# Optimization experiments

Hardware: AMD Instinct MI355X
Metric: run time of the kernel (lower is better)

The kernel has to match this reference:

```python
import jax, jax.numpy as jnp
import numpy as np

B, S, E = 8, 4096, 2048
LATENT, HEAD = 64, 128


def setup_inputs() -> dict:
    key = jax.random.key(0)
    ks = jax.random.split(key, 5)
    sd = lambda n: 1.0 / np.sqrt(n)
    return {
        "x": jax.random.normal(ks[0], (B, S, E), dtype=jnp.float32),
        "w_dkv": jax.random.normal(ks[1], (E, LATENT), dtype=jnp.float32) * sd(E),
        "w_k": jax.random.normal(ks[2], (LATENT, HEAD), dtype=jnp.float32) * sd(LATENT),
        "w_v": jax.random.normal(ks[3], (LATENT, HEAD), dtype=jnp.float32) * sd(LATENT),
        "w_q": jax.random.normal(ks[4], (E, HEAD), dtype=jnp.float32) * sd(E),
    }


def reference(x, w_dkv, w_k, w_v, w_q):
    # x: [B,S,E]. kv_cache=None path: cache = fresh compressed latents.
    latent = jnp.einsum('bse,el->bsl', x, w_dkv)          # [B,S,latent] compressed KV cache
    k = jnp.einsum('bsl,lh->bsh', latent, w_k)            # decompress keys   [B,S,head]
    v = jnp.einsum('bsl,lh->bsh', latent, w_v)            # decompress values [B,S,head]
    q = jnp.einsum('bse,eh->bsh', x, w_q)                 # queries [B,S,head]
    scale = w_q.shape[-1] ** -0.5
    scores = jnp.einsum('bqh,bkh->bqk', q, k) * scale     # [B,S,S]
    seq = x.shape[1]
    causal = jnp.tril(jnp.ones((seq, seq), dtype=bool))   # tril(seq, cache_len)
    scores = jnp.where(causal, scores, -jnp.inf)
    attn = jax.nn.softmax(scores, axis=-1)                # dropout p=0 (eval)
    out = jnp.einsum('bqk,bkh->bqh', attn, v)             # [B,S,head]
    return out, latent
```

## Files before the change

kernel.cpp:

```cpp
#include <hip/hip_runtime.h>

typedef __bf16 bf16;
typedef __bf16 bf16x2 __attribute__((ext_vector_type(2)));
typedef __bf16 bf16x4 __attribute__((ext_vector_type(4)));
typedef __bf16 bf16x8 __attribute__((ext_vector_type(8)));
typedef float  f32x4  __attribute__((ext_vector_type(4)));

#define MFMA16(a,b,c) __builtin_amdgcn_mfma_f32_16x16x32_bf16((a),(b),(c),0,0,0)

constexpr int Bn = 8, Sn = 4096, En = 2048, Ln = 64, Hn = 128;
constexpr int Mrows = Bn * Sn;

__device__ __forceinline__ void load_lds_16(const bf16* g, bf16* l) {
    __builtin_amdgcn_global_load_lds(
        (const __attribute__((address_space(1))) uint32_t*)g,
        (__attribute__((address_space(3))) uint32_t*)l, 16, 0, 0);
}

__global__ __launch_bounds__(256) void transpose_cvt(const float* __restrict__ in,
                                                     bf16* __restrict__ out,
                                                     int K, int N) {
    int tid = blockIdx.x * 256 + threadIdx.x;
    if (tid >= K * N) return;
    int k = tid / N, n = tid - k * N;
    out[n * K + k] = (bf16)in[tid];
}

__global__ __launch_bounds__(512) void gemm_xw(const float* __restrict__ x,
                                               const bf16* __restrict__ wT,
                                               const bf16* __restrict__ wkT,
                                               const bf16* __restrict__ wvT,
                                               float* __restrict__ latent_out,
                                               bf16* __restrict__ q_out,
                                               bf16* __restrict__ k_out,
                                               bf16* __restrict__ vT_out) {
    __shared__ __align__(16) bf16 As[64 * 72];
    __shared__ __align__(16) bf16 Bs[192 * 64];
    const int lane = threadIdx.x & 63;
    const int wave = threadIdx.x >> 6;
    const int col  = lane & 15, quad = lane >> 4;
    const int mgrp  = wave >> 1;
    const int nhalf = wave & 1;
    const int mblock = blockIdx.x * 64;

    f32x4 acc[6];
#pragma unroll
    for (int t = 0; t < 6; ++t) acc[t] = (f32x4){0.f, 0.f, 0.f, 0.f};

    const int bsub = lane >> 3;
    const int bkg0 = lane & 7;
    const int akc  = threadIdx.x & 15;
    const int arow0 = threadIdx.x >> 4;

    for (int step = 0; step < 32; ++step) {
        __syncthreads();
#pragma unroll
        for (int j = 0; j < 3; ++j) {
            int nr0 = wave * 24 + j * 8;
            int n = nr0 + bsub;
            int kgrp = bkg0 ^ bsub;
            const bf16* g = wT + (size_t)n * En + step * 64 + kgrp * 8;
            load_lds_16(g, &Bs[nr0 * 64]);
        }
#pragma unroll
        for (int p = 0; p < 2; ++p) {
            int row = p * 32 + arow0;
            f32x4 v = *(const f32x4*)(x + (size_t)(mblock + row) * En + step * 64 + akc * 4);
            bf16x4 c;
#pragma unroll
            for (int j = 0; j < 4; ++j) c[j] = (bf16)v[j];
            *(bf16x4*)(&As[row * 72 + akc * 4]) = c;
        }
        __syncthreads();
#pragma unroll
        for (int ks2 = 0; ks2 < 2; ++ks2) {
            bf16x8 a = *(const bf16x8*)(&As[(mgrp * 16 + col) * 72 + ks2 * 32 + quad * 8]);
#pragma unroll
            for (int t = 0; t < 6; ++t) {
                int n = nhalf * 96 + t * 16 + col;
                int sg = (ks2 * 4 + quad) ^ (col & 7);
                bf16x8 b = *(const bf16x8*)(&Bs[n * 64 + sg * 8]);
                acc[t] = MFMA16(a, b, acc[t]);
            }
        }
    }
    __syncthreads();
    if (nhalf == 0) {
#pragma unroll
        for (int t = 0; t < 4; ++t)
#pragma unroll
            for (int r = 0; r < 4; ++r)
                As[(mgrp * 16 + quad * 4 + r) * 72 + t * 16 + col] = (bf16)acc[t][r];
    }
#pragma unroll
    for (int t = 0; t < 6; ++t) {
        int gnt = nhalf * 6 + t;
#pragma unroll
        for (int r = 0; r < 4; ++r) {
            int row = mblock + mgrp * 16 + quad * 4 + r;
            if (gnt < 4) latent_out[(size_t)row * Ln + gnt * 16 + col] = acc[t][r];
            else         q_out[(size_t)row * Hn + (gnt - 4) * 16 + col] = (bf16)acc[t][r];
        }
    }
    __syncthreads();
    const bf16* w2 = (nhalf == 0) ? wkT : wvT;
    f32x4 kv[8];
#pragma unroll
    for (int nt = 0; nt < 8; ++nt) kv[nt] = (f32x4){0.f, 0.f, 0.f, 0.f};
#pragma unroll
    for (int ks = 0; ks < 2; ++ks) {
        bf16x8 a = *(const bf16x8*)(&As[(mgrp * 16 + col) * 72 + ks * 32 + quad * 8]);
#pragma unroll
        for (int nt = 0; nt < 8; ++nt) {
            bf16x8 b = *(const bf16x8*)(w2 + (nt * 16 + col) * Ln + ks * 32 + quad * 8);
            kv[nt] = MFMA16(a, b, kv[nt]);
        }
    }
    if (nhalf == 0) {
#pragma unroll
        for (int nt = 0; nt < 8; ++nt)
#pragma unroll
            for (int r = 0; r < 4; ++r) {
                int row = mblock + mgrp * 16 + quad * 4 + r;
                k_out[(size_t)row * Hn + nt * 16 + col] = (bf16)kv[nt][r];
            }
    } else {
        int bb = mblock >> 12;
        int sbase = (mblock & 4095) + mgrp * 16 + quad * 4;
#pragma unroll
        for (int nt = 0; nt < 8; ++nt) {
            bf16x4 pv;
#pragma unroll
            for (int r = 0; r < 4; ++r) pv[r] = (bf16)kv[nt][r];
            *(bf16x4*)(vT_out + ((size_t)bb * Hn + nt * 16 + col) * Sn + sbase) = pv;
        }
    }
}

__global__ __launch_bounds__(256, 2) void mla_attn(const bf16* __restrict__ qg,
                                                   const bf16* __restrict__ kg,
                                                   const bf16* __restrict__ vtg,
                                                   float* __restrict__ outg) {
    __shared__ __align__(16) bf16 Ks[2][64 * 128];
    __shared__ __align__(16) bf16 VtS[2][128 * 64];
    __shared__ __align__(16) bf16 Pb[4][16][72];
    const int lane = threadIdx.x & 63;
    const int wave = threadIdx.x >> 6;
    const int col  = lane & 15, quad = lane >> 4;
    const int rank  = blockIdx.x;
    const int qtile = 63 - (rank >> 3);
    const int bb    = rank & 7;
    const int qbase = qtile * 64;
    const bf16* kb  = kg  + (size_t)bb * Sn * Hn;
    const bf16* vbT = vtg + (size_t)bb * Sn * Hn;

    bf16x8 qf[4];
    {
        const bf16* qrow = qg + ((size_t)bb * Sn + qbase + wave * 16 + col) * Hn;
#pragma unroll
        for (int ks = 0; ks < 4; ++ks)
            qf[ks] = *(const bf16x8*)(qrow + ks * 32 + quad * 8);
    }
    f32x4 o[8];
#pragma unroll
    for (int t = 0; t < 8; ++t) o[t] = (f32x4){0.f, 0.f, 0.f, 0.f};
    float m_run = -3.0e38f;
    float l_run = 0.f;
    const float scale = 0.08838834764831845f;
    const int qrow = wave * 16 + col;

    auto stage = [&](int buf, int kt_) {
#pragma unroll
        for (int ii = 0; ii < 4; ++ii) {
            int i = wave * 4 + ii;
            int key = 4 * i + (lane >> 4);
            int p = lane & 15;
            int g = (p & 8) | ((p & 7) ^ (key & 7));
            load_lds_16(kb + (size_t)(kt_ * 64 + key) * Hn + g * 8, &Ks[buf][i * 512]);
        }
#pragma unroll
        for (int ii = 0; ii < 4; ++ii) {
            int i = wave * 4 + ii;
            int r = i * 8 + (lane >> 3);
            int cs = (lane & 7) ^ (r & 7);
            load_lds_16(vbT + (size_t)r * Sn + kt_ * 64 + cs * 8, &VtS[buf][i * 512]);
        }
    };

    stage(0, 0);
    for (int kt = 0; kt <= qtile; ++kt) {
        const int cur = kt & 1;
        if (kt < qtile) {
            stage(cur ^ 1, kt + 1);
            asm volatile("s_waitcnt vmcnt(8)" ::: "memory");
        } else {
            asm volatile("s_waitcnt vmcnt(0)" ::: "memory");
        }
        __builtin_amdgcn_s_barrier();
        __builtin_amdgcn_sched_barrier(0);
        const bf16* KsC = Ks[cur];
        const bf16* VtC = VtS[cur];

        f32x4 sa[4];
#pragma unroll
        for (int nt = 0; nt < 4; ++nt) {
            sa[nt] = (f32x4){0.f, 0.f, 0.f, 0.f};
#pragma unroll
            for (int ks = 0; ks < 4; ++ks) {
                int key = nt * 16 + col;
                int g = ks * 4 + quad;
                int pos = (g & 8) | ((g & 7) ^ (col & 7));
                bf16x8 kfr = *(const bf16x8*)(KsC + key * 128 + pos * 8);
                sa[nt] = MFMA16(kfr, qf[ks], sa[nt]);
            }
        }
        float p_[4][4];
        if (kt == qtile) {
#pragma unroll
            for (int nt = 0; nt < 4; ++nt)
#pragma unroll
                for (int r = 0; r < 4; ++r) {
                    float s = sa[nt][r] * scale;
                    if (nt * 16 + quad * 4 + r > qrow) s = -1.0e30f;
                    p_[nt][r] = s;
                }
        } else {
#pragma unroll
            for (int nt = 0; nt < 4; ++nt)
#pragma unroll
                for (int r = 0; r < 4; ++r) p_[nt][r] = sa[nt][r] * scale;
        }
        float mt = p_[0][0];
#pragma unroll
        for (int nt = 0; nt < 4; ++nt)
#pragma unroll
            for (int r = 0; r < 4; ++r) mt = fmaxf(mt, p_[nt][r]);
        mt = fmaxf(mt, __shfl_xor(mt, 16, 64));
        mt = fmaxf(mt, __shfl_xor(mt, 32, 64));
        float mn = fmaxf(m_run, mt);
        float alpha = __expf(m_run - mn);
        m_run = mn;
        float rs = 0.f;
#pragma unroll
        for (int nt = 0; nt < 4; ++nt)
#pragma unroll
            for (int r = 0; r < 4; ++r) {
                float p = __expf(p_[nt][r] - mn);
                p_[nt][r] = p;
                rs += p;
            }
        rs += __shfl_xor(rs, 16, 64);
        rs += __shfl_xor(rs, 32, 64);
        l_run = l_run * alpha + rs;
        float al[4];
#pragma unroll
        for (int r = 0; r < 4; ++r) al[r] = __shfl(alpha, quad * 4 + r, 64);
#pragma unroll
        for (int t = 0; t < 8; ++t)
#pragma unroll
            for (int r = 0; r < 4; ++r) o[t][r] *= al[r];
#pragma unroll
        for (int nt = 0; nt < 4; ++nt) {
            bf16x4 pv;
#pragma unroll
            for (int r = 0; r < 4; ++r) pv[r] = (bf16)p_[nt][r];
            *(bf16x4*)(&Pb[wave][col][((nt ^ (col >> 2)) & 3) * 16 + quad * 4]) = pv;
        }
#pragma unroll
        for (int ks = 0; ks < 2; ++ks) {
            int pos = (ks * 32 + quad * 8) ^ ((col >> 2) * 16);
            bf16x8 pa = *(const bf16x8*)(&Pb[wave][col][pos]);
#pragma unroll
            for (int nt = 0; nt < 8; ++nt) {
                int row = nt * 16 + col;
                int g = (ks * 4 + quad) ^ (row & 7);
                bf16x8 bv = *(const bf16x8*)(VtC + row * 64 + g * 8);
                o[nt] = MFMA16(pa, bv, o[nt]);
            }
        }
        __builtin_amdgcn_sched_barrier(0);
        __builtin_amdgcn_s_barrier();
    }
    float lr[4];
#pragma unroll
    for (int r = 0; r < 4; ++r) lr[r] = __shfl(l_run, quad * 4 + r, 64);
#pragma unroll
    for (int r = 0; r < 4; ++r) {
        float inv = 1.0f / lr[r];
        int row = qbase + wave * 16 + quad * 4 + r;
        float* orow = outg + ((size_t)bb * Sn + row) * Hn;
#pragma unroll
        for (int t = 0; t < 8; ++t)
            orow[t * 16 + col] = o[t][r] * inv;
    }
}

extern "C" void kernel_launch(void* const* d_in, const int* in_sizes, int n_in,
                              void* d_out, int out_size, void* d_ws, size_t ws_size,
                              hipStream_t stream) {
    const float* x     = (const float*)d_in[0];
    const float* w_dkv = (const float*)d_in[1];
    const float* w_k   = (const float*)d_in[2];
    const float* w_v   = (const float*)d_in[3];
    const float* w_q   = (const float*)d_in[4];

    float* out        = (float*)d_out;
    float* latent_out = out + (size_t)Mrows * Hn;

    char* ws = (char*)d_ws;
    bf16* q_ws = (bf16*)(ws);
    bf16* k_ws = (bf16*)(ws + (size_t)8  * 1024 * 1024);
    bf16* v_ws = (bf16*)(ws + (size_t)16 * 1024 * 1024);
    bf16* wT   = (bf16*)(ws + (size_t)24 * 1024 * 1024);
    bf16* wkT  = (bf16*)(ws + (size_t)24 * 1024 * 1024 + 768 * 1024);
    bf16* wvT  = (bf16*)(ws + (size_t)24 * 1024 * 1024 + 784 * 1024);

    transpose_cvt<<<(En * Ln + 255) / 256, 256, 0, stream>>>(w_dkv, wT, En, Ln);
    transpose_cvt<<<(En * Hn + 255) / 256, 256, 0, stream>>>(w_q, wT + (size_t)64 * En, En, Hn);
    transpose_cvt<<<(Ln * Hn + 255) / 256, 256, 0, stream>>>(w_k, wkT, Ln, Hn);
    transpose_cvt<<<(Ln * Hn + 255) / 256, 256, 0, stream>>>(w_v, wvT, Ln, Hn);
    gemm_xw<<<Mrows / 64, 512, 0, stream>>>(x, wT, wkT, wvT, latent_out, q_ws, k_ws, v_ws);
    mla_attn<<<Sn / 64 * Bn, 256, 0, stream>>>(q_ws, k_ws, v_ws, out);
}
```

Measured before the change: 510.7 us.

## Process two 16-row query subtiles per wave in attention, halve block size

The attention kernel now runs 2 waves per block instead of 4, and each wave handles 32 query rows as two 16-row subtiles. Each K and V fragment read from LDS feeds two MFMAs, which halves LDS read traffic per MFMA. Each wave now issues twice as many staging loads. The cost is roughly double the accumulator and softmax-state registers per wave, fewer waves per block to hide latency, and occupancy that now depends on launch_bounds(128,1).

```diff
diff --git a/kernel.cpp b/kernel.cpp
--- a/kernel.cpp
+++ b/kernel.cpp
@@ -137,13 +137,13 @@
     }
 }
 
-__global__ __launch_bounds__(256, 2) void mla_attn(const bf16* __restrict__ qg,
+__global__ __launch_bounds__(128, 1) void mla_attn(const bf16* __restrict__ qg,
                                                    const bf16* __restrict__ kg,
                                                    const bf16* __restrict__ vtg,
                                                    float* __restrict__ outg) {
     __shared__ __align__(16) bf16 Ks[2][64 * 128];
     __shared__ __align__(16) bf16 VtS[2][128 * 64];
-    __shared__ __align__(16) bf16 Pb[4][16][72];
+    __shared__ __align__(16) bf16 Pb[2][2][16][72];
     const int lane = threadIdx.x & 63;
     const int wave = threadIdx.x >> 6;
     const int col  = lane & 15, quad = lane >> 4;
@@ -154,33 +154,38 @@
     const bf16* kb  = kg  + (size_t)bb * Sn * Hn;
     const bf16* vbT = vtg + (size_t)bb * Sn * Hn;
 
-    bf16x8 qf[4];
+    bf16x8 qfA[4], qfB[4];
     {
-        const bf16* qrow = qg + ((size_t)bb * Sn + qbase + wave * 16 + col) * Hn;
-#pragma unroll
-        for (int ks = 0; ks < 4; ++ks)
-            qf[ks] = *(const bf16x8*)(qrow + ks * 32 + quad * 8);
-    }
-    f32x4 o[8];
-#pragma unroll
-    for (int t = 0; t < 8; ++t) o[t] = (f32x4){0.f, 0.f, 0.f, 0.f};
-    float m_run = -3.0e38f;
-    float l_run = 0.f;
+        const bf16* qr = qg + ((size_t)bb * Sn + qbase + wave * 32 + col) * Hn;
+#pragma unroll
+        for (int ks = 0; ks < 4; ++ks) {
+            qfA[ks] = *(const bf16x8*)(qr + ks * 32 + quad * 8);
+            qfB[ks] = *(const bf16x8*)(qr + 16 * Hn + ks * 32 + quad * 8);
+        }
+    }
+    f32x4 oA[8], oB[8];
+#pragma unroll
+    for (int t = 0; t < 8; ++t) {
+        oA[t] = (f32x4){0.f, 0.f, 0.f, 0.f};
+        oB[t] = (f32x4){0.f, 0.f, 0.f, 0.f};
+    }
+    float mA = -3.0e38f, mB = -3.0e38f, lA = 0.f, lB = 0.f;
     const float scale = 0.08838834764831845f;
-    const int qrow = wave * 16 + col;
+    const int qrA = wave * 32 + col;
+    const int qrB = qrA + 16;
 
     auto stage = [&](int buf, int kt_) {
 #pragma unroll
-        for (int ii = 0; ii < 4; ++ii) {
-            int i = wave * 4 + ii;
+        for (int ii = 0; ii < 8; ++ii) {
+            int i = wave * 8 + ii;
             int key = 4 * i + (lane >> 4);
             int p = lane & 15;
             int g = (p & 8) | ((p & 7) ^ (key & 7));
             load_lds_16(kb + (size_t)(kt_ * 64 + key) * Hn + g * 8, &Ks[buf][i * 512]);
         }
 #pragma unroll
-        for (int ii = 0; ii < 4; ++ii) {
-            int i = wave * 4 + ii;
+        for (int ii = 0; ii < 8; ++ii) {
+            int i = wave * 8 + ii;
             int r = i * 8 + (lane >> 3);
             int cs = (lane & 7) ^ (r & 7);
             load_lds_16(vbT + (size_t)r * Sn + kt_ * 64 + cs * 8, &VtS[buf][i * 512]);
@@ -192,7 +197,7 @@
         const int cur = kt & 1;
         if (kt < qtile) {
             stage(cur ^ 1, kt + 1);
-            asm volatile("s_waitcnt vmcnt(8)" ::: "memory");
+            asm volatile("s_waitcnt vmcnt(16)" ::: "memory");
         } else {
             asm volatile("s_waitcnt vmcnt(0)" ::: "memory");
         }
@@ -201,97 +206,130 @@
         const bf16* KsC = Ks[cur];
         const bf16* VtC = VtS[cur];
 
-        f32x4 sa[4];
+        f32x4 saA[4], saB[4];
 #pragma unroll
         for (int nt = 0; nt < 4; ++nt) {
-            sa[nt] = (f32x4){0.f, 0.f, 0.f, 0.f};
+            saA[nt] = (f32x4){0.f, 0.f, 0.f, 0.f};
+            saB[nt] = (f32x4){0.f, 0.f, 0.f, 0.f};
 #pragma unroll
             for (int ks = 0; ks < 4; ++ks) {
                 int key = nt * 16 + col;
                 int g = ks * 4 + quad;
                 int pos = (g & 8) | ((g & 7) ^ (col & 7));
                 bf16x8 kfr = *(const bf16x8*)(KsC + key * 128 + pos * 8);
-                sa[nt] = MFMA16(kfr, qf[ks], sa[nt]);
-            }
-        }
-        float p_[4][4];
+                saA[nt] = MFMA16(kfr, qfA[ks], saA[nt]);
+                saB[nt] = MFMA16(kfr, qfB[ks], saB[nt]);
+            }
+        }
+        float pA[4][4], pB[4][4];
         if (kt == qtile) {
 #pragma unroll
             for (int nt = 0; nt < 4; ++nt)
 #pragma unroll
                 for (int r = 0; r < 4; ++r) {
-                    float s = sa[nt][r] * scale;
-                    if (nt * 16 + quad * 4 + r > qrow) s = -1.0e30f;
-                    p_[nt][r] = s;
+                    int key = nt * 16 + quad * 4 + r;
+                    float sa_ = saA[nt][r] * scale;
+                    float sb_ = saB[nt][r] * scale;
+                    if (key > qrA) sa_ = -1.0e30f;
+                    if (key > qrB) sb_ = -1.0e30f;
+                    pA[nt][r] = sa_;
+                    pB[nt][r] = sb_;
                 }
         } else {
 #pragma unroll
             for (int nt = 0; nt < 4; ++nt)
 #pragma unroll
-                for (int r = 0; r < 4; ++r) p_[nt][r] = sa[nt][r] * scale;
-        }
-        float mt = p_[0][0];
+                for (int r = 0; r < 4; ++r) {
+                    pA[nt][r] = saA[nt][r] * scale;
+                    pB[nt][r] = saB[nt][r] * scale;
+                }
+        }
+        float mtA = pA[0][0], mtB = pB[0][0];
 #pragma unroll
         for (int nt = 0; nt < 4; ++nt)
 #pragma unroll
-            for (int r = 0; r < 4; ++r) mt = fmaxf(mt, p_[nt][r]);
-        mt = fmaxf(mt, __shfl_xor(mt, 16, 64));
-        mt = fmaxf(mt, __shfl_xor(mt, 32, 64));
-        float mn = fmaxf(m_run, mt);
-        float alpha = __expf(m_run - mn);
-        m_run = mn;
-        float rs = 0.f;
+            for (int r = 0; r < 4; ++r) {
+                mtA = fmaxf(mtA, pA[nt][r]);
+                mtB = fmaxf(mtB, pB[nt][r]);
+            }
+        mtA = fmaxf(mtA, __shfl_xor(mtA, 16, 64));
+        mtA = fmaxf(mtA, __shfl_xor(mtA, 32, 64));
+        mtB = fmaxf(mtB, __shfl_xor(mtB, 16, 64));
+        mtB = fmaxf(mtB, __shfl_xor(mtB, 32, 64));
+        float mnA = fmaxf(mA, mtA), mnB = fmaxf(mB, mtB);
+        float alphaA = __expf(mA - mnA), alphaB = __expf(mB - mnB);
+        mA = mnA; mB = mnB;
+        float rsA = 0.f, rsB = 0.f;
 #pragma unroll
         for (int nt = 0; nt < 4; ++nt)
 #pragma unroll
             for (int r = 0; r < 4; ++r) {
-                float p = __expf(p_[nt][r] - mn);
-                p_[nt][r] = p;
-                rs += p;
-            }
-        rs += __shfl_xor(rs, 16, 64);
-        rs += __shfl_xor(rs, 32, 64);
-        l_run = l_run * alpha + rs;
-        float al[4];
-#pragma unroll
-        for (int r = 0; r < 4; ++r) al[r] = __shfl(alpha, quad * 4 + r, 64);
+                float a = __expf(pA[nt][r] - mnA);
+                float b = __expf(pB[nt][r] - mnB);
+                pA[nt][r] = a; pB[nt][r] = b;
+                rsA += a; rsB += b;
+            }
+        rsA += __shfl_xor(rsA, 16, 64);
+        rsA += __shfl_xor(rsA, 32, 64);
+        rsB += __shfl_xor(rsB, 16, 64);
+        rsB += __shfl_xor(rsB, 32, 64);
+        lA = lA * alphaA + rsA;
+        lB = lB * alphaB + rsB;
+        float alA[4], alB[4];
+#pragma unroll
+        for (int r = 0; r < 4; ++r) {
+            alA[r] = __shfl(alphaA, quad * 4 + r, 64);
+            alB[r] = __shfl(alphaB, quad * 4 + r, 64);
+        }
 #pragma unroll
         for (int t = 0; t < 8; ++t)
 #pragma unroll
-            for (int r = 0; r < 4; ++r) o[t][r] *= al[r];
+            for (int r = 0; r < 4; ++r) {
+                oA[t][r] *= alA[r];
+                oB[t][r] *= alB[r];
+            }
 #pragma unroll
         for (int nt = 0; nt < 4; ++nt) {
-            bf16x4 pv;
-#pragma unroll
-            for (int r = 0; r < 4; ++r) pv[r] = (bf16)p_[nt][r];
-            *(bf16x4*)(&Pb[wave][col][((nt ^ (col >> 2)) & 3) * 16 + quad * 4]) = pv;
+            bf16x4 pva, pvb;
+#pragma unroll
+            for (int r = 0; r < 4; ++r) { pva[r] = (bf16)pA[nt][r]; pvb[r] = (bf16)pB[nt][r]; }
+            int cpos = ((nt ^ (col >> 2)) & 3) * 16 + quad * 4;
+            *(bf16x4*)(&Pb[wave][0][col][cpos]) = pva;
+            *(bf16x4*)(&Pb[wave][1][col][cpos]) = pvb;
         }
 #pragma unroll
         for (int ks = 0; ks < 2; ++ks) {
             int pos = (ks * 32 + quad * 8) ^ ((col >> 2) * 16);
-            bf16x8 pa = *(const bf16x8*)(&Pb[wave][col][pos]);
+            bf16x8 paA = *(const bf16x8*)(&Pb[wave][0][col][pos]);
+            bf16x8 paB = *(const bf16x8*)(&Pb[wave][1][col][pos]);
 #pragma unroll
             for (int nt = 0; nt < 8; ++nt) {
                 int row = nt * 16 + col;
                 int g = (ks * 4 + quad) ^ (row & 7);
                 bf16x8 bv = *(const bf16x8*)(VtC + row * 64 + g * 8);
-                o[nt] = MFMA16(pa, bv, o[nt]);
+                oA[nt] = MFMA16(paA, bv, oA[nt]);
+                oB[nt] = MFMA16(paB, bv, oB[nt]);
             }
         }
         __builtin_amdgcn_sched_barrier(0);
         __builtin_amdgcn_s_barrier();
     }
-    float lr[4];
-#pragma unroll
-    for (int r = 0; r < 4; ++r) lr[r] = __shfl(l_run, quad * 4 + r, 64);
+    float lrA[4], lrB[4];
 #pragma unroll
     for (int r = 0; r < 4; ++r) {
-        float inv = 1.0f / lr[r];
-        int row = qbase + wave * 16 + quad * 4 + r;
-        float* orow = outg + ((size_t)bb * Sn + row) * Hn;
-#pragma unroll
-        for (int t = 0; t < 8; ++t)
-            orow[t * 16 + col] = o[t][r] * inv;
+        lrA[r] = __shfl(lA, quad * 4 + r, 64);
+        lrB[r] = __shfl(lB, quad * 4 + r, 64);
+    }
+#pragma unroll
+    for (int r = 0; r < 4; ++r) {
+        float invA = 1.0f / lrA[r], invB = 1.0f / lrB[r];
+        int rowA = qbase + wave * 32 + quad * 4 + r;
+        float* oraw = outg + ((size_t)bb * Sn + rowA) * Hn;
+#pragma unroll
+        for (int t = 0; t < 8; ++t) {
+            oraw[t * 16 + col] = oA[t][r] * invA;
+            oraw[16 * Hn + t * 16 + col] = oB[t][r] * invB;
+        }
     }
 }
 
@@ -320,5 +358,5 @@
     transpose_cvt<<<(Ln * Hn + 255) / 256, 256, 0, stream>>>(w_k, wkT, Ln, Hn);
     transpose_cvt<<<(Ln * Hn + 255) / 256, 256, 0, stream>>>(w_v, wvT, Ln, Hn);
     gemm_xw<<<Mrows / 64, 512, 0, stream>>>(x, wT, wkT, wvT, latent_out, q_ws, k_ws, v_ws);
-    mla_attn<<<Sn / 64 * Bn, 256, 0, stream>>>(q_ws, k_ws, v_ws, out);
-}
+    mla_attn<<<Sn / 64 * Bn, 128, 0, stream>>>(q_ws, k_ws, v_ws, out);
+}
```

After: 557.1 us. +9.1%, slower.
